# Performance work log

Measured on AMD Instinct MI355X. Metric: run time of the kernel, lower is better.

Reference implementation:

```python
import jax, jax.numpy as jnp
import numpy as np
from itertools import combinations

D = 32
N_TRAIN = 50000
N_EVAL = 100000
LOG_2PI = float(np.log(2.0 * np.pi))


def setup_inputs() -> dict:
    key = jax.random.key(0)
    k1, k2 = jax.random.split(key)
    X_train = jax.random.normal(k1, (N_TRAIN, D), dtype=jnp.float32)
    x = jax.random.normal(k2, (N_EVAL, D), dtype=jnp.float32)
    return {"X_train": X_train, "x": x}


def reference(X_train, x):
    """GaussianPMIModel: train() then inv_exp_pmi_dict(x), with the dict's
    columns (null, singles, pairs in combinations order) stacked into one
    (N, 1 + D + C(D,2)) array. Null and singleton interactions are all-ones;
    each pair computes exp(logN_diag(x) - logN_full(x))."""
    d_feat = x.shape[1]
    # --- train(): empirical mean and covariance ---
    mean = jnp.mean(X_train, axis=0)                      # (D,)
    Xc = X_train - mean
    n = X_train.shape[0]
    cov = (Xc.T @ Xc) / (n - 1.0)                         # (D, D)

    # --- pair interactions (|subset| == 2), batched over all P pairs ---
    pairs = np.asarray(list(combinations(range(d_feat), 2)), dtype=np.int32)  # (P, 2)
    P = pairs.shape[0]
    xp = x[:, pairs]                                       # (N, P, 2) gather
    mp = mean[pairs]                                       # (P, 2)
    covp = cov[pairs[:, :, None], pairs[:, None, :]]       # (P, 2, 2)
    var = jnp.diagonal(covp, axis1=-2, axis2=-1)           # (P, 2)

    diff = xp - mp                                         # (N, P, 2)
    # MultivariateNormalDiag(loc=mean, scale_diag=sqrt(var)).log_prob
    lp_diag = (-0.5 * jnp.sum(diff * diff / var, axis=-1)
               - 0.5 * jnp.sum(jnp.log(var), axis=-1)
               - LOG_2PI)                                  # (N, P)

    # MultivariateNormalFullCovariance(loc=mean, cov=covp).log_prob via Cholesky
    L = jnp.linalg.cholesky(covp)                          # (P, 2, 2)
    b = jnp.moveaxis(diff, 0, -1)                          # (P, 2, N)
    z = jax.scipy.linalg.solve_triangular(L, b, lower=True)  # (P, 2, N)
    maha = jnp.sum(z * z, axis=1).T                        # (N, P)
    logdet = 2.0 * jnp.sum(jnp.log(jnp.diagonal(L, axis1=-2, axis2=-1)), axis=-1)  # (P,)
    lp_full = -0.5 * maha - 0.5 * logdet - LOG_2PI         # (N, P)

    pair_vals = jnp.exp(lp_diag - lp_full)                 # (N, P)
    ones = jnp.ones((x.shape[0], 1 + d_feat), dtype=x.dtype)  # null + singles
    return jnp.concatenate([ones, pair_vals], axis=1)      # (N, 1 + D + P)
```

## Files before the change

### kernel.cpp

```cpp
#include <hip/hip_runtime.h>
#include <math.h>


#define D       32
#define NPAIRS  496
#define NTRAIN  50000
#define NEVAL   100000
#define OUTC    529
#define ROWS_PB 16
#define COV_CHUNK 256
#define MEAN_CHUNK 512


__global__ void zero_ws_kernel(float* ws) {
    int t = blockIdx.x * blockDim.x + threadIdx.x;
    if (t < 560) ws[t] = 0.0f;
}

__global__ __launch_bounds__(256) void mean_kernel(const float* __restrict__ X,
                                                   float* __restrict__ ws) {
    __shared__ float sdata[256];
    int t = threadIdx.x;
    int col = t & 31;
    int rowoff = t >> 5;
    int base = blockIdx.x * MEAN_CHUNK;
    float s = 0.0f;
    for (int r = rowoff; r < MEAN_CHUNK; r += 8) {
        int row = base + r;
        if (row < NTRAIN) s += X[row * D + col];
    }
    sdata[t] = s;
    __syncthreads();
    if (t < 32) {
        float tot = 0.0f;
        #pragma unroll
        for (int w = 0; w < 8; ++w) tot += sdata[t + 32 * w];
        atomicAdd(&ws[t], tot);
    }
}

static __device__ __forceinline__ void emit_cov(float* ws, int i, int j, float v) {
    if (i > j) return;
    if (i == j) {
        atomicAdd(&ws[32 + i], v);
    } else {
        int p = i * 31 - (i * (i - 1)) / 2 + (j - i - 1);
        atomicAdd(&ws[64 + p], v);
    }
}

__global__ __launch_bounds__(256) void cov_kernel(const float* __restrict__ X,
                                                  float* __restrict__ ws) {
    __shared__ float xs[64 * D];
    __shared__ float smean[D];
    int t = threadIdx.x;
    if (t < D) smean[t] = ws[t] * (1.0f / NTRAIN);
    __syncthreads();

    int ti = t >> 4, tj = t & 15;
    float a00 = 0.f, a01 = 0.f, a10 = 0.f, a11 = 0.f;
    int base = blockIdx.x * COV_CHUNK;

    for (int tile = 0; tile < COV_CHUNK; tile += 64) {
        for (int e = t; e < 64 * D; e += 256) {
            int r = e >> 5, c = e & 31;
            int row = base + tile + r;
            xs[e] = (row < NTRAIN) ? (X[row * D + c] - smean[c]) : 0.0f;
        }
        __syncthreads();
        #pragma unroll 4
        for (int r = 0; r < 64; ++r) {
            float xi0 = xs[r * D + 2 * ti];
            float xi1 = xs[r * D + 2 * ti + 1];
            float xj0 = xs[r * D + 2 * tj];
            float xj1 = xs[r * D + 2 * tj + 1];
            a00 += xi0 * xj0; a01 += xi0 * xj1;
            a10 += xi1 * xj0; a11 += xi1 * xj1;
        }
        __syncthreads();
    }
    int i0 = 2 * ti, i1 = 2 * ti + 1, j0 = 2 * tj, j1 = 2 * tj + 1;
    emit_cov(ws, i0, j0, a00);
    emit_cov(ws, i0, j1, a01);
    emit_cov(ws, i1, j0, a10);
    emit_cov(ws, i1, j1, a11);
}

__global__ void prep_kernel(float* ws) {
    int t = threadIdx.x;
    if (t < D) ws[3040 + t] = ws[t] * (1.0f / NTRAIN);
    if (t < NPAIRS) {
        int i = 0, rem = t;
        while (rem >= 31 - i) { rem -= 31 - i; ++i; }
        int j = i + 1 + rem;
        const float inv_nm1 = 1.0f / (float)(NTRAIN - 1);
        float vi = ws[32 + i] * inv_nm1;
        float vj = ws[32 + j] * inv_nm1;
        float c  = ws[64 + t] * inv_nm1;
        float det = vi * vj - c * c;
        float invdet = 1.0f / det;
        ws[560  + t] = 0.5f * c * c * invdet / vi;
        ws[1056 + t] = 0.5f * c * c * invdet / vj;
        ws[1552 + t] = -c * invdet;
        ws[2048 + t] = 0.5f * logf(det / (vi * vj));
        ((int*)ws)[2544 + t] = i | (j << 8);
    }
}

__global__ __launch_bounds__(256) void pmi_kernel(const float* __restrict__ x,
                                                  const float* __restrict__ ws,
                                                  float* __restrict__ out) {
    __shared__ float cA[NPAIRS], cB[NPAIRS], cC[NPAIRS], cK[NPAIRS];
    __shared__ int   cIJ[NPAIRS];
    __shared__ float smean[D];
    __shared__ float dx[ROWS_PB * D];
    int t = threadIdx.x;

    for (int p = t; p < NPAIRS; p += 256) {
        cA[p]  = ws[560 + p];
        cB[p]  = ws[1056 + p];
        cC[p]  = ws[1552 + p];
        cK[p]  = ws[2048 + p];
        cIJ[p] = ((const int*)ws)[2544 + p];
    }
    if (t < D) smean[t] = ws[3040 + t];
    __syncthreads();

    int rowbase = blockIdx.x * ROWS_PB;
    for (int e = t; e < ROWS_PB * D; e += 256) {
        int r = e >> 5, c = e & 31;
        dx[e] = x[(size_t)(rowbase + r) * D + c] - smean[c];
    }
    __syncthreads();

    float4* out4 = (float4*)(out + (size_t)rowbase * OUTC);
    const int NF4 = ROWS_PB * OUTC / 4;
    for (int f = t; f < NF4; f += 256) {
        int e = 4 * f;
        int r = (int)((unsigned)e / OUTC);
        int k = e - r * OUTC;
        float v[4];
        #pragma unroll
        for (int q = 0; q < 4; ++q) {
            float val;
            if (k < 33) {
                val = 1.0f;
            } else {
                int p = k - 33;
                int ij = cIJ[p];
                int i = ij & 255, j = ij >> 8;
                float dxi = dx[r * D + i];
                float dxj = dx[r * D + j];
                val = __expf(cA[p] * dxi * dxi + cB[p] * dxj * dxj +
                             cC[p] * dxi * dxj + cK[p]);
            }
            v[q] = val;
            if (++k == OUTC) { k = 0; ++r; }
        }
        out4[f] = make_float4(v[0], v[1], v[2], v[3]);
    }
}

extern "C" void kernel_launch(void* const* d_in, const int* in_sizes, int n_in,
                              void* d_out, int out_size, void* d_ws, size_t ws_size,
                              hipStream_t stream) {
    const float* X = (const float*)d_in[0];
    const float* x = (const float*)d_in[1];
    float* out = (float*)d_out;
    float* ws  = (float*)d_ws;

    hipLaunchKernelGGL(zero_ws_kernel, dim3(3), dim3(256), 0, stream, ws);
    hipLaunchKernelGGL(mean_kernel, dim3((NTRAIN + MEAN_CHUNK - 1) / MEAN_CHUNK),
                       dim3(256), 0, stream, X, ws);
    hipLaunchKernelGGL(cov_kernel, dim3((NTRAIN + COV_CHUNK - 1) / COV_CHUNK),
                       dim3(256), 0, stream, X, ws);
    hipLaunchKernelGGL(prep_kernel, dim3(1), dim3(512), 0, stream, ws);
    hipLaunchKernelGGL(pmi_kernel, dim3(NEVAL / ROWS_PB), dim3(256), 0, stream,
                       x, ws, out);
}
```

Baseline: 310.0 us.

## Keep per-column pair coefficients in registers and stream rows with nontemporal stores

The PMI kernel now gives each thread fixed output columns. The pair coefficients for those columns (pre-scaled by log2e so exp2f can be used) stay in registers instead of being read from shared-memory tables for every element. Each block now handles 50 rows: it loads x with float4 reads and writes each output row as scalar nontemporal stores, replacing the per-element divide and modulo indexing. Null and singleton columns come out as exp2(0)=1 through zero coefficients. The covariance kernel switches to float2 LDS reads and a smaller chunk size, which doubles its atomic traffic. The scalar stores give up float4 vectorisation, and with 529 columns per row the writes are not 16-byte aligned.

```diff
diff --git a/kernel.cpp b/kernel.cpp
--- a/kernel.cpp
+++ b/kernel.cpp
@@ -7,8 +7,8 @@
 #define NTRAIN  50000
 #define NEVAL   100000
 #define OUTC    529
-#define ROWS_PB 16
-#define COV_CHUNK 256
+#define ROWS_PB 50
+#define COV_CHUNK 128
 #define MEAN_CHUNK 512
 
 
@@ -60,6 +60,7 @@
     int ti = t >> 4, tj = t & 15;
     float a00 = 0.f, a01 = 0.f, a10 = 0.f, a11 = 0.f;
     int base = blockIdx.x * COV_CHUNK;
+    const float2* xs2 = (const float2*)xs;
 
     for (int tile = 0; tile < COV_CHUNK; tile += 64) {
         for (int e = t; e < 64 * D; e += 256) {
@@ -70,12 +71,10 @@
         __syncthreads();
         #pragma unroll 4
         for (int r = 0; r < 64; ++r) {
-            float xi0 = xs[r * D + 2 * ti];
-            float xi1 = xs[r * D + 2 * ti + 1];
-            float xj0 = xs[r * D + 2 * tj];
-            float xj1 = xs[r * D + 2 * tj + 1];
-            a00 += xi0 * xj0; a01 += xi0 * xj1;
-            a10 += xi1 * xj0; a11 += xi1 * xj1;
+            float2 xi = xs2[r * 16 + ti];
+            float2 xj = xs2[r * 16 + tj];
+            a00 += xi.x * xj.x; a01 += xi.x * xj.y;
+            a10 += xi.y * xj.x; a11 += xi.y * xj.y;
         }
         __syncthreads();
     }
@@ -107,57 +106,68 @@
     }
 }
 
+struct Coef { float A, B, C, K; int oi, oj; };
+
+static __device__ __forceinline__ Coef load_coef(const float* __restrict__ ws, int c) {
+    const float LOG2E = 1.44269504088896340736f;
+    Coef k;
+    if (c < 33) {
+        k.A = 0.f; k.B = 0.f; k.C = 0.f; k.K = 0.f; k.oi = 0; k.oj = 0;
+    } else {
+        int p = c - 33;
+        k.A = ws[560  + p] * LOG2E;
+        k.B = ws[1056 + p] * LOG2E;
+        k.C = ws[1552 + p] * LOG2E;
+        k.K = ws[2048 + p] * LOG2E;
+        int ij = ((const int*)ws)[2544 + p];
+        k.oi = ij & 255; k.oj = ij >> 8;
+    }
+    return k;
+}
+
+static __device__ __forceinline__ float pair_val(const Coef& k,
+                                                 const float* __restrict__ dxr) {
+    float di = dxr[k.oi];
+    float dj = dxr[k.oj];
+    float e = fmaf(k.A, di * di, fmaf(k.B, dj * dj, fmaf(k.C, di * dj, k.K)));
+    return exp2f(e);
+}
+
 __global__ __launch_bounds__(256) void pmi_kernel(const float* __restrict__ x,
                                                   const float* __restrict__ ws,
                                                   float* __restrict__ out) {
-    __shared__ float cA[NPAIRS], cB[NPAIRS], cC[NPAIRS], cK[NPAIRS];
-    __shared__ int   cIJ[NPAIRS];
     __shared__ float smean[D];
     __shared__ float dx[ROWS_PB * D];
     int t = threadIdx.x;
+    if (t < D) smean[t] = ws[3040 + t];
 
-    for (int p = t; p < NPAIRS; p += 256) {
-        cA[p]  = ws[560 + p];
-        cB[p]  = ws[1056 + p];
-        cC[p]  = ws[1552 + p];
-        cK[p]  = ws[2048 + p];
-        cIJ[p] = ((const int*)ws)[2544 + p];
-    }
-    if (t < D) smean[t] = ws[3040 + t];
+    Coef c0 = load_coef(ws, t);
+    Coef c1 = load_coef(ws, t + 256);
+    bool has3 = (t + 512) < OUTC;
+    Coef c2 = load_coef(ws, has3 ? t + 512 : 0);
     __syncthreads();
 
     int rowbase = blockIdx.x * ROWS_PB;
-    for (int e = t; e < ROWS_PB * D; e += 256) {
-        int r = e >> 5, c = e & 31;
-        dx[e] = x[(size_t)(rowbase + r) * D + c] - smean[c];
+    const float4* x4 = (const float4*)(x + (size_t)rowbase * D);
+    float4* dx4 = (float4*)dx;
+    for (int f = t; f < ROWS_PB * D / 4; f += 256) {
+        float4 v = x4[f];
+        int cb = (f & 7) * 4;
+        v.x -= smean[cb];     v.y -= smean[cb + 1];
+        v.z -= smean[cb + 2]; v.w -= smean[cb + 3];
+        dx4[f] = v;
     }
     __syncthreads();
 
-    float4* out4 = (float4*)(out + (size_t)rowbase * OUTC);
-    const int NF4 = ROWS_PB * OUTC / 4;
-    for (int f = t; f < NF4; f += 256) {
-        int e = 4 * f;
-        int r = (int)((unsigned)e / OUTC);
-        int k = e - r * OUTC;
-        float v[4];
-        #pragma unroll
-        for (int q = 0; q < 4; ++q) {
-            float val;
-            if (k < 33) {
-                val = 1.0f;
-            } else {
-                int p = k - 33;
-                int ij = cIJ[p];
-                int i = ij & 255, j = ij >> 8;
-                float dxi = dx[r * D + i];
-                float dxj = dx[r * D + j];
-                val = __expf(cA[p] * dxi * dxi + cB[p] * dxj * dxj +
-                             cC[p] * dxi * dxj + cK[p]);
-            }
-            v[q] = val;
-            if (++k == OUTC) { k = 0; ++r; }
-        }
-        out4[f] = make_float4(v[0], v[1], v[2], v[3]);
+    float* orow = out + (size_t)rowbase * OUTC;
+    const float* dxr = dx;
+    #pragma unroll 2
+    for (int r = 0; r < ROWS_PB; ++r) {
+        __builtin_nontemporal_store(pair_val(c0, dxr), &orow[t]);
+        __builtin_nontemporal_store(pair_val(c1, dxr), &orow[t + 256]);
+        if (has3)
+            __builtin_nontemporal_store(pair_val(c2, dxr), &orow[t + 512]);
+        orow += OUTC; dxr += D;
     }
 }
 
```

New measurement: 367.1 us. 1.18x slower.
